# Performance work log

Hardware: AMD Instinct MI355X
Metric: run time of the kernel (lower is better)

The kernel has to match this reference:

```python
import jax, jax.numpy as jnp
import numpy as np


def gcn_conv(x, edge_index, W, b):
    # PyG GCNConv: h = x @ W; add self-loops; symmetric D^-1/2 (A+I) D^-1/2 aggregation; + bias
    n = x.shape[0]
    h = x @ W  # [N, out]
    loop = jnp.arange(n, dtype=edge_index.dtype)
    src = jnp.concatenate([edge_index[0], loop])  # message sources
    dst = jnp.concatenate([edge_index[1], loop])  # message targets
    ones = jnp.ones(dst.shape[0], dtype=h.dtype)
    deg = jax.ops.segment_sum(ones, dst, num_segments=n)  # in-degree incl. self-loop
    dinv = jnp.where(deg > 0, jax.lax.rsqrt(deg), 0.0)
    norm = dinv[src] * dinv[dst]  # [E+N]
    msg = h[src] * norm[:, None]  # gather + scale
    out = jax.ops.segment_sum(msg, dst, num_segments=n)  # scatter-add
    return out + b


def setup_inputs() -> dict:
    key = jax.random.key(0)
    ks = jax.random.split(key, 6)
    N, E, D = 100000, 600000, 128
    x = jax.random.normal(ks[0], (N, D), dtype=jnp.float32)
    edge_index = jax.random.randint(ks[1], (2, E), 0, N, dtype=jnp.int64)
    s = 1.0 / np.sqrt(D)
    W1 = jax.random.normal(ks[2], (D, D), dtype=jnp.float32) * s
    b1 = jnp.zeros((D,), dtype=jnp.float32)
    W2 = jax.random.normal(ks[3], (2 * D, D), dtype=jnp.float32) * (1.0 / np.sqrt(2 * D))
    b2 = jnp.zeros((D,), dtype=jnp.float32)
    Wout = jax.random.normal(ks[4], (D, 1), dtype=jnp.float32) * s
    bout = jnp.zeros((1,), dtype=jnp.float32)
    return {"x": x, "edge_index": edge_index, "W1": W1, "b1": b1,
            "W2": W2, "b2": b2, "Wout": Wout, "bout": bout}


def reference(x, edge_index, W1, b1, W2, b2, Wout, bout):
    y = gcn_conv(x, edge_index, W1, b1)          # [N, D]
    y = jnp.concatenate([x, y], axis=-1)          # [N, 2D]
    y = jax.nn.leaky_relu(y, negative_slope=0.01)
    z = gcn_conv(y, edge_index, W2, b2)           # [N, D]
    z = jax.nn.leaky_relu(z, negative_slope=0.01)
    return z @ Wout + bout                        # [N, 1]
```

## Files before the change

### kernel.cpp

```cpp
#include <hip/hip_runtime.h>

#define DIM 128
#define CAP 48

typedef _Float16 half8 __attribute__((ext_vector_type(8)));
typedef float f32x4 __attribute__((ext_vector_type(4)));

__device__ __forceinline__ float lrelu(float v) { return v > 0.f ? v : 0.01f * v; }

__global__ __launch_bounds__(256) void k_prep(
    const int* __restrict__ src, const int* __restrict__ dst,
    int* __restrict__ cursor, int* __restrict__ srcs, int e, int eb,
    const float* __restrict__ W1, _Float16* __restrict__ Wp1,
    const float* __restrict__ W2, _Float16* __restrict__ Wp2) {
    int b = blockIdx.x;
    if (b < eb) {
        int i = b * 256 + threadIdx.x;
        if (i < e) {
            int d = dst[i];
            int p = atomicAdd(&cursor[d], 1);
            if (p < CAP) srcs[(size_t)d * CAP + p] = src[i];
        }
        return;
    }
    b -= eb;
    const float* W;
    _Float16* Wp;
    int tid2;
    if (b < 64) { W = W1; Wp = Wp1; tid2 = b * 256 + threadIdx.x; }
    else        { W = W2; Wp = Wp2; tid2 = (b - 64) * 256 + threadIdx.x; }
    int jj = tid2 & 7;
    int frag = tid2 >> 3;
    int l = frag & 63;
    int cb = (frag >> 6) & 7;
    int kb = frag >> 9;
    int k = kb * 32 + ((l >> 4) << 3) + jj;
    int nn = cb * 16 + (l & 15);
    Wp[tid2] = (_Float16)W[(size_t)k * DIM + nn];
}

__global__ __launch_bounds__(256, 2) void k_mm1(
    const float* __restrict__ x, const _Float16* __restrict__ Wp1,
    const _Float16* __restrict__ Wp2, const int* __restrict__ cursor,
    _Float16* __restrict__ hs, _Float16* __restrict__ P, int n) {
    __shared__ _Float16 Hs[64 * 136];
    const int tid = threadIdx.x;
    const int w = tid >> 6, l = tid & 63;
    const int row0 = blockIdx.x * 64;
    const int arow = row0 + w * 16 + (l & 15);
    const int kq = (l >> 4) << 3;
    const bool ok = arow < n;
    const float* xr = &x[(size_t)arow * DIM + kq];

    f32x4 ah[8], ap[8];
#pragma unroll
    for (int cb = 0; cb < 8; ++cb) {
        f32x4 z = {0.f, 0.f, 0.f, 0.f};
        ah[cb] = z; ap[cb] = z;
    }

#pragma unroll
    for (int kb = 0; kb < 4; ++kb) {
        float4 v0 = make_float4(0.f, 0.f, 0.f, 0.f), v1 = v0;
        if (ok) {
            v0 = *(const float4*)&xr[kb * 32];
            v1 = *(const float4*)&xr[kb * 32 + 4];
        }
        half8 a, al;
        a[0] = (_Float16)v0.x; a[1] = (_Float16)v0.y;
        a[2] = (_Float16)v0.z; a[3] = (_Float16)v0.w;
        a[4] = (_Float16)v1.x; a[5] = (_Float16)v1.y;
        a[6] = (_Float16)v1.z; a[7] = (_Float16)v1.w;
#pragma unroll
        for (int e = 0; e < 8; ++e) {
            _Float16 t = a[e];
            al[e] = (t > (_Float16)0.f) ? t : t * (_Float16)0.01f;
        }
#pragma unroll
        for (int cb = 0; cb < 8; ++cb) {
            half8 bf = *(const half8*)&Wp1[((kb * 8 + cb) * 64 + l) * 8];
            ah[cb] = __builtin_amdgcn_mfma_f32_16x16x32_f16(a, bf, ah[cb], 0, 0, 0);
        }
#pragma unroll
        for (int cb = 0; cb < 8; ++cb) {
            half8 bf = *(const half8*)&Wp2[((kb * 8 + cb) * 64 + l) * 8];
            ap[cb] = __builtin_amdgcn_mfma_f32_16x16x32_f16(al, bf, ap[cb], 0, 0, 0);
        }
    }
    const int orow = w * 16 + ((l >> 4) << 2);
    const int oc = l & 15;
#pragma unroll
    for (int reg = 0; reg < 4; ++reg) {
        int grow = row0 + orow + reg;
        float d = (grow < n) ? rsqrtf((float)cursor[grow] + 1.0f) : 0.f;
#pragma unroll
        for (int cb = 0; cb < 8; ++cb)
            Hs[(orow + reg) * 136 + cb * 16 + oc] = (_Float16)(ah[cb][reg] * d);
    }
    __syncthreads();
#pragma unroll
    for (int it = 0; it < 4; ++it) {
        int i = it * 256 + tid;
        int r = i >> 4, c = (i & 15) * 8;
        if (row0 + r < n)
            *(half8*)&hs[(size_t)(row0 + r) * DIM + c] = *(const half8*)&Hs[r * 136 + c];
    }
    _Float16* pl = P + ((size_t)(blockIdx.x * 4 + w) * 64 + l) * 32;
#pragma unroll
    for (int c = 0; c < 4; ++c) {
        half8 o;
#pragma unroll
        for (int e = 0; e < 4; ++e) {
            o[e]     = (_Float16)ap[2 * c][e];
            o[4 + e] = (_Float16)ap[2 * c + 1][e];
        }
        *(half8*)&pl[c * 8] = o;
    }
}

__global__ __launch_bounds__(256, 2) void k_mm2g(
    const _Float16* __restrict__ hs, const int* __restrict__ cursor,
    const int* __restrict__ srcs, const float* __restrict__ b1,
    const _Float16* __restrict__ Wp2, const _Float16* __restrict__ P,
    _Float16* __restrict__ hs2, int n) {
    __shared__ _Float16 LS[64 * 136];
    const int tid = threadIdx.x;
    const int w = tid >> 6, l = tid & 63;
    const int g = tid & 15, gid = tid >> 4;
    const int row0 = blockIdx.x * 64;

    f32x4 acc[8];
    const _Float16* pl = P + ((size_t)(blockIdx.x * 4 + w) * 64 + l) * 32;
#pragma unroll
    for (int c = 0; c < 4; ++c) {
        half8 pv = *(const half8*)&pl[c * 8];
#pragma unroll
        for (int e = 0; e < 4; ++e) {
            acc[2 * c][e]     = (float)pv[e];
            acc[2 * c + 1][e] = (float)pv[4 + e];
        }
    }

#pragma unroll
    for (int it = 0; it < 4; ++it) {
        int node = row0 + it * 16 + gid;
        half8 o = 0;
        if (node < n) {
            int rawc = cursor[node];
            int cnt = rawc > CAP ? CAP : rawc;
            const int* sl = &srcs[(size_t)node * CAP];
            half8 h = *(const half8*)&hs[(size_t)node * DIM + g * 8];
            float a[8];
#pragma unroll
            for (int e = 0; e < 8; ++e) a[e] = (float)h[e];
            for (int base = 0; base < cnt; base += 16) {
                int m = cnt - base;
                if (m > 16) m = 16;
                int sidb = (g < m) ? sl[base + g] : 0;
                int j = 0;
                for (; j + 4 <= m; j += 4) {
                    int s0 = __shfl(sidb, j, 16);
                    int s1 = __shfl(sidb, j + 1, 16);
                    int s2 = __shfl(sidb, j + 2, 16);
                    int s3 = __shfl(sidb, j + 3, 16);
                    half8 v0 = *(const half8*)&hs[(size_t)s0 * DIM + g * 8];
                    half8 v1 = *(const half8*)&hs[(size_t)s1 * DIM + g * 8];
                    half8 v2 = *(const half8*)&hs[(size_t)s2 * DIM + g * 8];
                    half8 v3 = *(const half8*)&hs[(size_t)s3 * DIM + g * 8];
#pragma unroll
                    for (int e = 0; e < 8; ++e)
                        a[e] += (float)v0[e] + (float)v1[e] + (float)v2[e] + (float)v3[e];
                }
                for (; j + 2 <= m; j += 2) {
                    int s0 = __shfl(sidb, j, 16);
                    int s1 = __shfl(sidb, j + 1, 16);
                    half8 v0 = *(const half8*)&hs[(size_t)s0 * DIM + g * 8];
                    half8 v1 = *(const half8*)&hs[(size_t)s1 * DIM + g * 8];
#pragma unroll
                    for (int e = 0; e < 8; ++e) a[e] += (float)v0[e] + (float)v1[e];
                }
                if (j < m) {
                    int s0 = __shfl(sidb, j, 16);
                    half8 v0 = *(const half8*)&hs[(size_t)s0 * DIM + g * 8];
#pragma unroll
                    for (int e = 0; e < 8; ++e) a[e] += (float)v0[e];
                }
            }
            float d = rsqrtf((float)rawc + 1.0f);
            const float4 bb0 = *(const float4*)&b1[g * 8];
            const float4 bb1 = *(const float4*)&b1[g * 8 + 4];
            o[0] = (_Float16)lrelu(fmaf(a[0], d, bb0.x));
            o[1] = (_Float16)lrelu(fmaf(a[1], d, bb0.y));
            o[2] = (_Float16)lrelu(fmaf(a[2], d, bb0.z));
            o[3] = (_Float16)lrelu(fmaf(a[3], d, bb0.w));
            o[4] = (_Float16)lrelu(fmaf(a[4], d, bb1.x));
            o[5] = (_Float16)lrelu(fmaf(a[5], d, bb1.y));
            o[6] = (_Float16)lrelu(fmaf(a[6], d, bb1.z));
            o[7] = (_Float16)lrelu(fmaf(a[7], d, bb1.w));
        }
        *(half8*)&LS[(((it * 4 + (g >> 2)) * 64) + (g & 3) * 16 + gid) * 8] = o;
    }
    __syncthreads();

#pragma unroll
    for (int kb = 0; kb < 4; ++kb) {
        half8 a = *(const half8*)&LS[((w * 4 + kb) * 64 + l) * 8];
#pragma unroll
        for (int cb = 0; cb < 8; ++cb) {
            half8 bf = *(const half8*)&Wp2[(((kb + 4) * 8 + cb) * 64 + l) * 8];
            acc[cb] = __builtin_amdgcn_mfma_f32_16x16x32_f16(a, bf, acc[cb], 0, 0, 0);
        }
    }
    __syncthreads();
    const int orow = w * 16 + ((l >> 4) << 2);
    const int oc = l & 15;
#pragma unroll
    for (int reg = 0; reg < 4; ++reg) {
        int grow = row0 + orow + reg;
        float d = (grow < n) ? rsqrtf((float)cursor[grow] + 1.0f) : 0.f;
#pragma unroll
        for (int cb = 0; cb < 8; ++cb)
            LS[(orow + reg) * 136 + cb * 16 + oc] = (_Float16)(acc[cb][reg] * d);
    }
    __syncthreads();
#pragma unroll
    for (int it = 0; it < 4; ++it) {
        int i = it * 256 + tid;
        int r = i >> 4, c = (i & 15) * 8;
        if (row0 + r < n)
            *(half8*)&hs2[(size_t)(row0 + r) * DIM + c] = *(const half8*)&LS[r * 136 + c];
    }
}

__global__ __launch_bounds__(256) void k_gather2(
    const _Float16* __restrict__ hs2, const int* __restrict__ cursor,
    const int* __restrict__ srcs, const float* __restrict__ b2,
    const float* __restrict__ wout, const float* __restrict__ bout,
    float* __restrict__ out, int n) {
    const int node = blockIdx.x * 16 + (threadIdx.x >> 4);
    const int g = threadIdx.x & 15;
    if (node >= n) return;
    int rawc = cursor[node];
    int cnt = rawc > CAP ? CAP : rawc;
    const int* sl = &srcs[(size_t)node * CAP];
    half8 h = *(const half8*)&hs2[(size_t)node * DIM + g * 8];
    float a[8];
#pragma unroll
    for (int e = 0; e < 8; ++e) a[e] = (float)h[e];
    for (int base = 0; base < cnt; base += 16) {
        int m = cnt - base;
        if (m > 16) m = 16;
        int sidb = (g < m) ? sl[base + g] : 0;
        int j = 0;
        for (; j + 4 <= m; j += 4) {
            int s0 = __shfl(sidb, j, 16);
            int s1 = __shfl(sidb, j + 1, 16);
            int s2 = __shfl(sidb, j + 2, 16);
            int s3 = __shfl(sidb, j + 3, 16);
            half8 v0 = *(const half8*)&hs2[(size_t)s0 * DIM + g * 8];
            half8 v1 = *(const half8*)&hs2[(size_t)s1 * DIM + g * 8];
            half8 v2 = *(const half8*)&hs2[(size_t)s2 * DIM + g * 8];
            half8 v3 = *(const half8*)&hs2[(size_t)s3 * DIM + g * 8];
#pragma unroll
            for (int e = 0; e < 8; ++e)
                a[e] += (float)v0[e] + (float)v1[e] + (float)v2[e] + (float)v3[e];
        }
        for (; j + 2 <= m; j += 2) {
            int s0 = __shfl(sidb, j, 16);
            int s1 = __shfl(sidb, j + 1, 16);
            half8 v0 = *(const half8*)&hs2[(size_t)s0 * DIM + g * 8];
            half8 v1 = *(const half8*)&hs2[(size_t)s1 * DIM + g * 8];
#pragma unroll
            for (int e = 0; e < 8; ++e) a[e] += (float)v0[e] + (float)v1[e];
        }
        if (j < m) {
            int s0 = __shfl(sidb, j, 16);
            half8 v0 = *(const half8*)&hs2[(size_t)s0 * DIM + g * 8];
#pragma unroll
            for (int e = 0; e < 8; ++e) a[e] += (float)v0[e];
        }
    }
    float d = rsqrtf((float)rawc + 1.0f);
    const float4 bb0 = *(const float4*)&b2[g * 8];
    const float4 bb1 = *(const float4*)&b2[g * 8 + 4];
    const float4 wv0 = *(const float4*)&wout[g * 8];
    const float4 wv1 = *(const float4*)&wout[g * 8 + 4];
    float s = lrelu(fmaf(a[0], d, bb0.x)) * wv0.x + lrelu(fmaf(a[1], d, bb0.y)) * wv0.y +
              lrelu(fmaf(a[2], d, bb0.z)) * wv0.z + lrelu(fmaf(a[3], d, bb0.w)) * wv0.w +
              lrelu(fmaf(a[4], d, bb1.x)) * wv1.x + lrelu(fmaf(a[5], d, bb1.y)) * wv1.y +
              lrelu(fmaf(a[6], d, bb1.z)) * wv1.z + lrelu(fmaf(a[7], d, bb1.w)) * wv1.w;
#pragma unroll
    for (int off = 8; off > 0; off >>= 1) s += __shfl_down(s, off, 16);
    if (g == 0) out[node] = s + bout[0];
}

extern "C" void kernel_launch(void* const* d_in, const int* in_sizes, int n_in,
                              void* d_out, int out_size, void* d_ws, size_t ws_size,
                              hipStream_t stream) {
    const float* x    = (const float*)d_in[0];
    const int*   ei   = (const int*)d_in[1];
    const float* W1   = (const float*)d_in[2];
    const float* b1   = (const float*)d_in[3];
    const float* W2   = (const float*)d_in[4];
    const float* b2   = (const float*)d_in[5];
    const float* Wout = (const float*)d_in[6];
    const float* bout = (const float*)d_in[7];
    float* out = (float*)d_out;

    const int N = in_sizes[0] / DIM;
    const int E = in_sizes[1] / 2;
    const int* src = ei;
    const int* dst = ei + E;

    const int gb = (N + 63) / 64;
    const long long nx = (long long)N * DIM;

    size_t Na = ((size_t)N + 63) & ~(size_t)63;
    int* cursor   = (int*)d_ws;
    int* srcs     = cursor + Na;
    _Float16* Wp1 = (_Float16*)(srcs + (size_t)N * CAP);
    _Float16* Wp2 = Wp1 + 128 * 128;
    _Float16* hsb = Wp2 + 256 * 128;
    _Float16* Pb  = hsb + nx;

    const int eb = (E + 255) / 256;

    hipMemsetAsync(cursor, 0, (size_t)N * sizeof(int), stream);
    k_prep<<<eb + 192, 256, 0, stream>>>(src, dst, cursor, srcs, E, eb, W1, Wp1, W2, Wp2);
    k_mm1<<<gb, 256, 0, stream>>>(x, Wp1, Wp2, cursor, hsb, Pb, N);
    k_mm2g<<<gb, 256, 0, stream>>>(hsb, cursor, srcs, b1, Wp2, Pb, Pb, N);
    k_gather2<<<(N + 15) / 16, 256, 0, stream>>>(Pb, cursor, srcs, b2, Wout, bout, out, N);
}
```

Before: 230.2 us.

## Fuse four kernels into one persistent cooperative kernel with grid syncs

Merges the prep, first matmul, aggregate+second matmul, and final gather kernels into a single cooperative persistent kernel that loops over tiles and separates phases with grid-wide syncs. This removes three kernel launch boundaries and their tail drain. The cost is a persistent grid sized from occupancy (3 blocks per CU requested), which may limit latency hiding in the gather phases and adds grid.sync overhead. A fallback to the original four launches is kept if the cooperative launch fails.

```diff
diff --git a/kernel.cpp b/kernel.cpp
--- a/kernel.cpp
+++ b/kernel.cpp
@@ -1,4 +1,7 @@
 #include <hip/hip_runtime.h>
+#include <hip/hip_cooperative_groups.h>
+
+namespace cg = cooperative_groups;
 
 #define DIM 128
 #define CAP 48
@@ -8,14 +11,14 @@
 
 __device__ __forceinline__ float lrelu(float v) { return v > 0.f ? v : 0.01f * v; }
 
-__global__ __launch_bounds__(256) void k_prep(
-    const int* __restrict__ src, const int* __restrict__ dst,
+
+__device__ __forceinline__ void phase1_body(
+    int b, int tid, const int* __restrict__ src, const int* __restrict__ dst,
     int* __restrict__ cursor, int* __restrict__ srcs, int e, int eb,
-    const float* __restrict__ W1, _Float16* __restrict__ Wp1,
-    const float* __restrict__ W2, _Float16* __restrict__ Wp2) {
-    int b = blockIdx.x;
+    const float* __restrict__ W1, const float* __restrict__ W2,
+    _Float16* __restrict__ Wp1, _Float16* __restrict__ Wp2) {
     if (b < eb) {
-        int i = b * 256 + threadIdx.x;
+        int i = b * 256 + tid;
         if (i < e) {
             int d = dst[i];
             int p = atomicAdd(&cursor[d], 1);
@@ -23,30 +26,28 @@
         }
         return;
     }
-    b -= eb;
+    int bb = b - eb;
     const float* W;
     _Float16* Wp;
     int tid2;
-    if (b < 64) { W = W1; Wp = Wp1; tid2 = b * 256 + threadIdx.x; }
-    else        { W = W2; Wp = Wp2; tid2 = (b - 64) * 256 + threadIdx.x; }
+    if (bb < 64) { W = W1; Wp = Wp1; tid2 = bb * 256 + tid; }
+    else         { W = W2; Wp = Wp2; tid2 = (bb - 64) * 256 + tid; }
     int jj = tid2 & 7;
     int frag = tid2 >> 3;
-    int l = frag & 63;
+    int ll = frag & 63;
     int cb = (frag >> 6) & 7;
     int kb = frag >> 9;
-    int k = kb * 32 + ((l >> 4) << 3) + jj;
-    int nn = cb * 16 + (l & 15);
+    int k = kb * 32 + ((ll >> 4) << 3) + jj;
+    int nn = cb * 16 + (ll & 15);
     Wp[tid2] = (_Float16)W[(size_t)k * DIM + nn];
 }
 
-__global__ __launch_bounds__(256, 2) void k_mm1(
-    const float* __restrict__ x, const _Float16* __restrict__ Wp1,
+__device__ __forceinline__ void phase2_body(
+    int t, int tid, const float* __restrict__ x, const _Float16* __restrict__ Wp1,
     const _Float16* __restrict__ Wp2, const int* __restrict__ cursor,
-    _Float16* __restrict__ hs, _Float16* __restrict__ P, int n) {
-    __shared__ _Float16 Hs[64 * 136];
-    const int tid = threadIdx.x;
+    _Float16* __restrict__ hs, _Float16* __restrict__ P, int n, _Float16* LS) {
     const int w = tid >> 6, l = tid & 63;
-    const int row0 = blockIdx.x * 64;
+    const int row0 = t * 64;
     const int arow = row0 + w * 16 + (l & 15);
     const int kq = (l >> 4) << 3;
     const bool ok = arow < n;
@@ -58,7 +59,6 @@
         f32x4 z = {0.f, 0.f, 0.f, 0.f};
         ah[cb] = z; ap[cb] = z;
     }
-
 #pragma unroll
     for (int kb = 0; kb < 4; ++kb) {
         float4 v0 = make_float4(0.f, 0.f, 0.f, 0.f), v1 = v0;
@@ -72,9 +72,9 @@
         a[4] = (_Float16)v1.x; a[5] = (_Float16)v1.y;
         a[6] = (_Float16)v1.z; a[7] = (_Float16)v1.w;
 #pragma unroll
-        for (int e = 0; e < 8; ++e) {
-            _Float16 t = a[e];
-            al[e] = (t > (_Float16)0.f) ? t : t * (_Float16)0.01f;
+        for (int ee = 0; ee < 8; ++ee) {
+            _Float16 tt = a[ee];
+            al[ee] = (tt > (_Float16)0.f) ? tt : tt * (_Float16)0.01f;
         }
 #pragma unroll
         for (int cb = 0; cb < 8; ++cb) {
@@ -87,6 +87,7 @@
             ap[cb] = __builtin_amdgcn_mfma_f32_16x16x32_f16(al, bf, ap[cb], 0, 0, 0);
         }
     }
+    __syncthreads();
     const int orow = w * 16 + ((l >> 4) << 2);
     const int oc = l & 15;
 #pragma unroll
@@ -95,7 +96,7 @@
         float d = (grow < n) ? rsqrtf((float)cursor[grow] + 1.0f) : 0.f;
 #pragma unroll
         for (int cb = 0; cb < 8; ++cb)
-            Hs[(orow + reg) * 136 + cb * 16 + oc] = (_Float16)(ah[cb][reg] * d);
+            LS[(orow + reg) * 136 + cb * 16 + oc] = (_Float16)(ah[cb][reg] * d);
     }
     __syncthreads();
 #pragma unroll
@@ -103,44 +104,41 @@
         int i = it * 256 + tid;
         int r = i >> 4, c = (i & 15) * 8;
         if (row0 + r < n)
-            *(half8*)&hs[(size_t)(row0 + r) * DIM + c] = *(const half8*)&Hs[r * 136 + c];
-    }
-    _Float16* pl = P + ((size_t)(blockIdx.x * 4 + w) * 64 + l) * 32;
+            *(half8*)&hs[(size_t)(row0 + r) * DIM + c] = *(const half8*)&LS[r * 136 + c];
+    }
+    _Float16* pl = P + ((size_t)(t * 4 + w) * 64 + l) * 32;
 #pragma unroll
     for (int c = 0; c < 4; ++c) {
         half8 o;
 #pragma unroll
-        for (int e = 0; e < 4; ++e) {
-            o[e]     = (_Float16)ap[2 * c][e];
-            o[4 + e] = (_Float16)ap[2 * c + 1][e];
+        for (int ee = 0; ee < 4; ++ee) {
+            o[ee]     = (_Float16)ap[2 * c][ee];
+            o[4 + ee] = (_Float16)ap[2 * c + 1][ee];
         }
         *(half8*)&pl[c * 8] = o;
     }
 }
 
-__global__ __launch_bounds__(256, 2) void k_mm2g(
-    const _Float16* __restrict__ hs, const int* __restrict__ cursor,
+__device__ __forceinline__ void phase3_body(
+    int t, int tid, const _Float16* __restrict__ hs, const int* __restrict__ cursor,
     const int* __restrict__ srcs, const float* __restrict__ b1,
-    const _Float16* __restrict__ Wp2, const _Float16* __restrict__ P,
-    _Float16* __restrict__ hs2, int n) {
-    __shared__ _Float16 LS[64 * 136];
-    const int tid = threadIdx.x;
+    const _Float16* __restrict__ Wp2, _Float16* P, int n, _Float16* LS) {
     const int w = tid >> 6, l = tid & 63;
+    const int row0 = t * 64;
     const int g = tid & 15, gid = tid >> 4;
-    const int row0 = blockIdx.x * 64;
 
     f32x4 acc[8];
-    const _Float16* pl = P + ((size_t)(blockIdx.x * 4 + w) * 64 + l) * 32;
+    const _Float16* pl = P + ((size_t)(t * 4 + w) * 64 + l) * 32;
 #pragma unroll
     for (int c = 0; c < 4; ++c) {
         half8 pv = *(const half8*)&pl[c * 8];
 #pragma unroll
-        for (int e = 0; e < 4; ++e) {
-            acc[2 * c][e]     = (float)pv[e];
-            acc[2 * c + 1][e] = (float)pv[4 + e];
-        }
-    }
-
+        for (int ee = 0; ee < 4; ++ee) {
+            acc[2 * c][ee]     = (float)pv[ee];
+            acc[2 * c + 1][ee] = (float)pv[4 + ee];
+        }
+    }
+    __syncthreads();
 #pragma unroll
     for (int it = 0; it < 4; ++it) {
         int node = row0 + it * 16 + gid;
@@ -152,7 +150,7 @@
             half8 h = *(const half8*)&hs[(size_t)node * DIM + g * 8];
             float a[8];
 #pragma unroll
-            for (int e = 0; e < 8; ++e) a[e] = (float)h[e];
+            for (int ee = 0; ee < 8; ++ee) a[ee] = (float)h[ee];
             for (int base = 0; base < cnt; base += 16) {
                 int m = cnt - base;
                 if (m > 16) m = 16;
@@ -168,8 +166,8 @@
                     half8 v2 = *(const half8*)&hs[(size_t)s2 * DIM + g * 8];
                     half8 v3 = *(const half8*)&hs[(size_t)s3 * DIM + g * 8];
 #pragma unroll
-                    for (int e = 0; e < 8; ++e)
-                        a[e] += (float)v0[e] + (float)v1[e] + (float)v2[e] + (float)v3[e];
+                    for (int ee = 0; ee < 8; ++ee)
+                        a[ee] += (float)v0[ee] + (float)v1[ee] + (float)v2[ee] + (float)v3[ee];
                 }
                 for (; j + 2 <= m; j += 2) {
                     int s0 = __shfl(sidb, j, 16);
@@ -177,13 +175,13 @@
                     half8 v0 = *(const half8*)&hs[(size_t)s0 * DIM + g * 8];
                     half8 v1 = *(const half8*)&hs[(size_t)s1 * DIM + g * 8];
 #pragma unroll
-                    for (int e = 0; e < 8; ++e) a[e] += (float)v0[e] + (float)v1[e];
+                    for (int ee = 0; ee < 8; ++ee) a[ee] += (float)v0[ee] + (float)v1[ee];
                 }
                 if (j < m) {
                     int s0 = __shfl(sidb, j, 16);
                     half8 v0 = *(const half8*)&hs[(size_t)s0 * DIM + g * 8];
 #pragma unroll
-                    for (int e = 0; e < 8; ++e) a[e] += (float)v0[e];
+                    for (int ee = 0; ee < 8; ++ee) a[ee] += (float)v0[ee];
                 }
             }
             float d = rsqrtf((float)rawc + 1.0f);
@@ -201,7 +199,6 @@
         *(half8*)&LS[(((it * 4 + (g >> 2)) * 64) + (g & 3) * 16 + gid) * 8] = o;
     }
     __syncthreads();
-
 #pragma unroll
     for (int kb = 0; kb < 4; ++kb) {
         half8 a = *(const half8*)&LS[((w * 4 + kb) * 64 + l) * 8];
@@ -228,17 +225,17 @@
         int i = it * 256 + tid;
         int r = i >> 4, c = (i & 15) * 8;
         if (row0 + r < n)
-            *(half8*)&hs2[(size_t)(row0 + r) * DIM + c] = *(const half8*)&LS[r * 136 + c];
-    }
-}
-
-__global__ __launch_bounds__(256) void k_gather2(
-    const _Float16* __restrict__ hs2, const int* __restrict__ cursor,
+            *(half8*)&P[(size_t)(row0 + r) * DIM + c] = *(const half8*)&LS[r * 136 + c];
+    }
+}
+
+__device__ __forceinline__ void phase4_body(
+    int gr, int tid, const _Float16* __restrict__ hs2, const int* __restrict__ cursor,
     const int* __restrict__ srcs, const float* __restrict__ b2,
     const float* __restrict__ wout, const float* __restrict__ bout,
     float* __restrict__ out, int n) {
-    const int node = blockIdx.x * 16 + (threadIdx.x >> 4);
-    const int g = threadIdx.x & 15;
+    const int node = gr * 16 + (tid >> 4);
+    const int g = tid & 15;
     if (node >= n) return;
     int rawc = cursor[node];
     int cnt = rawc > CAP ? CAP : rawc;
@@ -246,7 +243,7 @@
     half8 h = *(const half8*)&hs2[(size_t)node * DIM + g * 8];
     float a[8];
 #pragma unroll
-    for (int e = 0; e < 8; ++e) a[e] = (float)h[e];
+    for (int ee = 0; ee < 8; ++ee) a[ee] = (float)h[ee];
     for (int base = 0; base < cnt; base += 16) {
         int m = cnt - base;
         if (m > 16) m = 16;
@@ -262,8 +259,8 @@
             half8 v2 = *(const half8*)&hs2[(size_t)s2 * DIM + g * 8];
             half8 v3 = *(const half8*)&hs2[(size_t)s3 * DIM + g * 8];
 #pragma unroll
-            for (int e = 0; e < 8; ++e)
-                a[e] += (float)v0[e] + (float)v1[e] + (float)v2[e] + (float)v3[e];
+            for (int ee = 0; ee < 8; ++ee)
+                a[ee] += (float)v0[ee] + (float)v1[ee] + (float)v2[ee] + (float)v3[ee];
         }
         for (; j + 2 <= m; j += 2) {
             int s0 = __shfl(sidb, j, 16);
@@ -271,13 +268,13 @@
             half8 v0 = *(const half8*)&hs2[(size_t)s0 * DIM + g * 8];
             half8 v1 = *(const half8*)&hs2[(size_t)s1 * DIM + g * 8];
 #pragma unroll
-            for (int e = 0; e < 8; ++e) a[e] += (float)v0[e] + (float)v1[e];
+            for (int ee = 0; ee < 8; ++ee) a[ee] += (float)v0[ee] + (float)v1[ee];
         }
         if (j < m) {
             int s0 = __shfl(sidb, j, 16);
             half8 v0 = *(const half8*)&hs2[(size_t)s0 * DIM + g * 8];
 #pragma unroll
-            for (int e = 0; e < 8; ++e) a[e] += (float)v0[e];
+            for (int ee = 0; ee < 8; ++ee) a[ee] += (float)v0[ee];
         }
     }
     float d = rsqrtf((float)rawc + 1.0f);
@@ -292,6 +289,62 @@
 #pragma unroll
     for (int off = 8; off > 0; off >>= 1) s += __shfl_down(s, off, 16);
     if (g == 0) out[node] = s + bout[0];
+}
+
+
+__global__ __launch_bounds__(256, 3) void k_all(
+    const float* __restrict__ x, const int* __restrict__ src, const int* __restrict__ dst,
+    int* __restrict__ cursor, int* __restrict__ srcs,
+    const float* __restrict__ W1, const float* __restrict__ W2,
+    _Float16* __restrict__ Wp1, _Float16* __restrict__ Wp2,
+    _Float16* __restrict__ hs, _Float16* P,
+    const float* __restrict__ b1, const float* __restrict__ b2,
+    const float* __restrict__ wout, const float* __restrict__ bout,
+    float* __restrict__ out, int n, int e, int eb, int gb) {
+    cg::grid_group grid = cg::this_grid();
+    __shared__ _Float16 LS[64 * 136];
+    const int tid = threadIdx.x;
+    const int NB = gridDim.x;
+
+    for (int b = blockIdx.x; b < eb + 192; b += NB)
+        phase1_body(b, tid, src, dst, cursor, srcs, e, eb, W1, W2, Wp1, Wp2);
+    grid.sync();
+    for (int t = blockIdx.x; t < gb; t += NB)
+        phase2_body(t, tid, x, Wp1, Wp2, cursor, hs, P, n, LS);
+    grid.sync();
+    for (int t = blockIdx.x; t < gb; t += NB)
+        phase3_body(t, tid, hs, cursor, srcs, b1, Wp2, P, n, LS);
+    grid.sync();
+    const int ng = (n + 15) >> 4;
+    for (int gr = blockIdx.x; gr < ng; gr += NB)
+        phase4_body(gr, tid, P, cursor, srcs, b2, wout, bout, out, n);
+}
+
+
+__global__ __launch_bounds__(256) void k_prep(
+    const int* src, const int* dst, int* cursor, int* srcs, int e, int eb,
+    const float* W1, _Float16* Wp1, const float* W2, _Float16* Wp2) {
+    phase1_body(blockIdx.x, threadIdx.x, src, dst, cursor, srcs, e, eb, W1, W2, Wp1, Wp2);
+}
+
+__global__ __launch_bounds__(256, 2) void k_mm1(
+    const float* x, const _Float16* Wp1, const _Float16* Wp2,
+    const int* cursor, _Float16* hs, _Float16* P, int n) {
+    __shared__ _Float16 LS[64 * 136];
+    phase2_body(blockIdx.x, threadIdx.x, x, Wp1, Wp2, cursor, hs, P, n, LS);
+}
+
+__global__ __launch_bounds__(256, 2) void k_mm2g(
+    const _Float16* hs, const int* cursor, const int* srcs, const float* b1,
+    const _Float16* Wp2, _Float16* P, int n) {
+    __shared__ _Float16 LS[64 * 136];
+    phase3_body(blockIdx.x, threadIdx.x, hs, cursor, srcs, b1, Wp2, P, n, LS);
+}
+
+__global__ __launch_bounds__(256) void k_gather2(
+    const _Float16* hs2, const int* cursor, const int* srcs, const float* b2,
+    const float* wout, const float* bout, float* out, int n) {
+    phase4_body(blockIdx.x, threadIdx.x, hs2, cursor, srcs, b2, wout, bout, out, n);
 }
 
 extern "C" void kernel_launch(void* const* d_in, const int* in_sizes, int n_in,
@@ -313,6 +366,7 @@
     const int* dst = ei + E;
 
     const int gb = (N + 63) / 64;
+    const int eb = (E + 255) / 256;
     const long long nx = (long long)N * DIM;
 
     size_t Na = ((size_t)N + 63) & ~(size_t)63;
@@ -323,11 +377,31 @@
     _Float16* hsb = Wp2 + 256 * 128;
     _Float16* Pb  = hsb + nx;
 
-    const int eb = (E + 255) / 256;
-
-    hipMemsetAsync(cursor, 0, (size_t)N * sizeof(int), stream);
-    k_prep<<<eb + 192, 256, 0, stream>>>(src, dst, cursor, srcs, E, eb, W1, Wp1, W2, Wp2);
-    k_mm1<<<gb, 256, 0, stream>>>(x, Wp1, Wp2, cursor, hsb, Pb, N);
-    k_mm2g<<<gb, 256, 0, stream>>>(hsb, cursor, srcs, b1, Wp2, Pb, Pb, N);
-    k_gather2<<<(N + 15) / 16, 256, 0, stream>>>(Pb, cursor, srcs, b2, Wout, bout, out, N);
-}
+    (void)hipMemsetAsync(cursor, 0, (size_t)N * sizeof(int), stream);
+
+    int occ = 0, nCU = 0;
+    hipError_t e1 = hipOccupancyMaxActiveBlocksPerMultiprocessor(&occ, (const void*)k_all, 256, 0);
+    hipError_t e2 = hipDeviceGetAttribute(&nCU, hipDeviceAttributeMultiprocessorCount, 0);
+    hipError_t lerr = hipErrorUnknown;
+    if (e1 == hipSuccess && e2 == hipSuccess && occ > 0 && nCU > 0) {
+        int grid = occ * nCU;
+        void* args[] = {
+            (void*)&x, (void*)&src, (void*)&dst,
+            (void*)&cursor, (void*)&srcs,
+            (void*)&W1, (void*)&W2,
+            (void*)&Wp1, (void*)&Wp2,
+            (void*)&hsb, (void*)&Pb,
+            (void*)&b1, (void*)&b2,
+            (void*)&Wout, (void*)&bout,
+            (void*)&out, (void*)&N, (void*)&E, (void*)&eb, (void*)&gb
+        };
+        lerr = hipLaunchCooperativeKernel((const void*)k_all, dim3(grid), dim3(256),
+                                          args, 0, stream);
+    }
+    if (lerr != hipSuccess) {
+        k_prep<<<eb + 192, 256, 0, stream>>>(src, dst, cursor, srcs, E, eb, W1, Wp1, W2, Wp2);
+        k_mm1<<<gb, 256, 0, stream>>>(x, Wp1, Wp2, cursor, hsb, Pb, N);
+        k_mm2g<<<gb, 256, 0, stream>>>(hsb, cursor, srcs, b1, Wp2, Pb, N);
+        k_gather2<<<(N + 15) / 16, 256, 0, stream>>>(Pb, cursor, srcs, b2, Wout, bout, out, N);
+    }
+}
```

Measured after the change: 499.3 us. +117.0%, slower.
